# Performance work log

Measured on AMD Instinct MI355X. Metric: run time of the kernel, lower is better.

Reference implementation:

```python
import jax, jax.numpy as jnp
import numpy as np

B, N_TOK, C = 16, 4096, 512
TIME_DIM = 512
H_HEADS, WS = 8, 8
HEAD_DIM = C // H_HEADS
RES = 64  # sqrt(N_TOK)
NH = NW = RES // WS
SCALE = HEAD_DIM ** -0.5


def _rel_pos_index(ws):
    coords = np.stack(np.meshgrid(np.arange(ws), np.arange(ws), indexing='ij'))  # (2,ws,ws)
    flat = coords.reshape(2, -1)  # (2, ws*ws)
    rel = flat[:, :, None] - flat[:, None, :]  # (2, N, N)
    rel = rel.transpose(1, 2, 0).astype(np.int64)
    rel[:, :, 0] += ws - 1
    rel[:, :, 1] += ws - 1
    rel[:, :, 0] *= 2 * ws - 1
    return rel.sum(-1)  # (ws*ws, ws*ws)

REL_IDX = jnp.asarray(_rel_pos_index(WS))


def setup_inputs() -> dict:
    key = jax.random.key(0)
    ks = jax.random.split(key, 9)
    return {
        'x': jax.random.normal(ks[0], (B, N_TOK, C), jnp.float32),
        'time_emb': jax.random.normal(ks[1], (B, TIME_DIM), jnp.float32),
        'Wqkv': jax.random.normal(ks[2], (3 * C, C), jnp.float32) * 0.02,
        'bqkv': jnp.zeros((3 * C,), jnp.float32),
        'Wt': jax.random.normal(ks[3], (3 * C, TIME_DIM), jnp.float32) * 0.02,
        'bt': jnp.zeros((3 * C,), jnp.float32),
        'Wo': jax.random.normal(ks[4], (C, C), jnp.float32) * 0.02,
        'bo': jnp.zeros((C,), jnp.float32),
        'bias_table': jax.random.normal(ks[5], ((2 * WS - 1) ** 2, H_HEADS), jnp.float32) * 0.02,
    }


def reference(x, time_emb, Wqkv, bqkv, Wt, bt, Wo, bo, bias_table):
    Bo = x.shape[0]
    # window partition: (B, H*W, C) -> (B*nH*nW, ws*ws, C)
    xw = x.reshape(Bo, NH, WS, NW, WS, C).transpose(0, 1, 3, 2, 4, 5).reshape(-1, WS * WS, C)
    Bw, N = xw.shape[0], WS * WS
    # time emb broadcast to every window: (Bw, time_dim)
    te = jnp.broadcast_to(time_emb[:, None, :], (Bo, NH * NW, TIME_DIM)).reshape(Bw, TIME_DIM)
    # spatial qkv: (Bw, N, 3, h, d) -> q/k/v (Bw, h, N, d)
    qkv_s = (xw @ Wqkv.T + bqkv).reshape(Bw, N, 3, H_HEADS, HEAD_DIM).transpose(2, 0, 3, 1, 4)
    # time qkv: (Bw, 3, h, d) -> (3, Bw, h, 1, d)
    qkv_t = (te @ Wt.T + bt).reshape(Bw, 1, 3, H_HEADS, HEAD_DIM).transpose(2, 0, 3, 1, 4)
    q = qkv_s[0] + qkv_t[0]
    k = qkv_s[1] + qkv_t[1]
    v = qkv_s[2] + qkv_t[2]
    # relative position bias: (h, N, N)
    bias = bias_table[REL_IDX.reshape(-1)].reshape(N, N, H_HEADS).transpose(2, 0, 1)
    attn = jnp.einsum('bhnd,bhmd->bhnm', q, k) * SCALE + bias[None]
    attn = jax.nn.softmax(attn, axis=-1)
    out = jnp.einsum('bhnm,bhmd->bhnd', attn, v)
    out = out.transpose(0, 2, 1, 3).reshape(Bw, N, C)
    out = out @ Wo.T + bo
    # NOTE: source module's unpartition condition (ws^2 < ws^2) is False -> stays windowed
    return out
```

## Files before the change

kernel.cpp:

```cpp
#include <hip/hip_runtime.h>

using u16 = unsigned short;
typedef __bf16 bf16x8 __attribute__((ext_vector_type(8)));
typedef float floatx4 __attribute__((ext_vector_type(4)));

__device__ __forceinline__ u16 f2bf(float f) {
    union { float f; unsigned u; } v; v.f = f;
    unsigned r = v.u + 0x7fffu + ((v.u >> 16) & 1u);
    return (u16)(r >> 16);
}

__device__ __forceinline__ void gld16(const void* g, void* l) {
    __builtin_amdgcn_global_load_lds(
        (const __attribute__((address_space(1))) void*)g,
        (__attribute__((address_space(3))) void*)l, 16, 0, 0);
}

__device__ __forceinline__ void cvt4(const float* __restrict__ src,
                                     u16* __restrict__ dst, int i) {
    float4 v = *(const float4*)(src + i);
    ushort4 o;
    o.x = f2bf(v.x); o.y = f2bf(v.y); o.z = f2bf(v.z); o.w = f2bf(v.w);
    *(ushort4*)(dst + i) = o;
}

__global__ __launch_bounds__(256) void prep_k(
    const float* __restrict__ x, const float* __restrict__ Wqkv,
    const float* __restrict__ Wo, const float* __restrict__ te,
    const float* __restrict__ Wt, const float* __restrict__ bt,
    const float* __restrict__ btab,
    u16* __restrict__ xbf, u16* __restrict__ wqkvbf, u16* __restrict__ wobf,
    float* __restrict__ qkvt, float* __restrict__ biasf)
{
    const int b = blockIdx.x, tid = threadIdx.x;
    if (b < 768) {
        cvt4(Wqkv, wqkvbf, b * 1024 + tid * 4);
    } else if (b < 1024) {
        cvt4(Wo, wobf, (b - 768) * 1024 + tid * 4);
    } else if (b < 1120) {
        const int bb = b - 1024;
        const int batch = bb / 6;
        const int c = (bb % 6) * 256 + tid;
        const float4* a4 = (const float4*)(te + batch * 512);
        const float4* w4 = (const float4*)(Wt + (size_t)c * 512);
        float s = 0.f;
        for (int i = 0; i < 128; ++i) {
            float4 av = a4[i], wv = w4[i];
            s += av.x * wv.x + av.y * wv.y + av.z * wv.z + av.w * wv.w;
        }
        qkvt[batch * 1536 + c] = s + bt[c];
    } else if (b < 1152) {
        const int e0 = (b - 1120) * 1024 + tid;
        for (int k = 0; k < 4; ++k) {
            int e = e0 + k * 256;
            int h = e >> 12, rc = e & 4095, row = rc >> 6, col = rc & 63;
            int idx = ((row >> 3) - (col >> 3) + 7) * 15 + ((row & 7) - (col & 7) + 7);
            biasf[e] = btab[idx * 8 + h];
        }
    } else {
        const int base = (b - 1152) * 4096 + tid * 4;
        for (int k = 0; k < 4; ++k) cvt4(x, xbf, base + k * 1024);
    }
}

__global__ __launch_bounds__(256, 3) void gemm_qkv_k(
    const u16* __restrict__ A, const u16* __restrict__ B,
    const float* __restrict__ bqkv, const float* __restrict__ qkvt,
    u16* __restrict__ C)
{
    __shared__ __align__(16) u16 lA[128 * 32];
    __shared__ __align__(16) u16 lB[128 * 32];
    const int tid = threadIdx.x;
    const int lane = tid & 63, wv = tid >> 6;
    const int ln = lane & 15, quad = lane >> 4;
    const int tn = blockIdx.x, tm = blockIdx.y;
    const int wm = (wv & 1) * 64, wn = (wv >> 1) * 64;

    floatx4 acc[4][4];
#pragma unroll
    for (int i = 0; i < 4; ++i)
#pragma unroll
        for (int j = 0; j < 4; ++j) acc[i][j] = (floatx4){0.f, 0.f, 0.f, 0.f};

    const int srow = tid >> 2, scb = tid & 3;
    const u16* ag = A + (size_t)(tm * 128 + srow) * 512 + scb * 8;
    const u16* bg = B + (size_t)(tn * 128 + srow) * 512 + scb * 8;
    u16* la0 = &lA[tid * 8];
    u16* la1 = &lA[2048 + tid * 8];
    u16* lb0 = &lB[tid * 8];
    u16* lb1 = &lB[2048 + tid * 8];

    for (int k0 = 0; k0 < 512; k0 += 32) {
        __syncthreads();
        gld16(ag + k0, la0);
        gld16(ag + 64 * 512 + k0, la1);
        gld16(bg + k0, lb0);
        gld16(bg + 64 * 512 + k0, lb1);
        __syncthreads();
        bf16x8 af[4], bf[4];
#pragma unroll
        for (int mt = 0; mt < 4; ++mt)
            af[mt] = *(const bf16x8*)&lA[(wm + mt * 16 + ln) * 32 + quad * 8];
#pragma unroll
        for (int nt = 0; nt < 4; ++nt)
            bf[nt] = *(const bf16x8*)&lB[(wn + nt * 16 + ln) * 32 + quad * 8];
#pragma unroll
        for (int mt = 0; mt < 4; ++mt)
#pragma unroll
            for (int nt = 0; nt < 4; ++nt)
                acc[mt][nt] = __builtin_amdgcn_mfma_f32_16x16x32_bf16(
                    af[mt], bf[nt], acc[mt][nt], 0, 0, 0);
    }

    const float* qt = qkvt + (tm >> 5) * 1536;
#pragma unroll
    for (int nt = 0; nt < 4; ++nt) {
        const int col = tn * 128 + wn + nt * 16 + ln;
        const float add = bqkv[col] + qt[col];
#pragma unroll
        for (int mt = 0; mt < 4; ++mt) {
            const int row0 = tm * 128 + wm + mt * 16 + quad * 4;
#pragma unroll
            for (int r = 0; r < 4; ++r)
                C[(size_t)(row0 + r) * 1536 + col] = f2bf(acc[mt][nt][r] + add);
        }
    }
}

__global__ __launch_bounds__(256, 2) void attn_k(
    const u16* __restrict__ qkv, const float* __restrict__ biasf,
    u16* __restrict__ aout)
{
    __shared__ __align__(16) u16 vt[4][64 * 72];
    __shared__ __align__(16) u16 pl[4][64 * 72];
    const int tid = threadIdx.x, lane = tid & 63, wv = tid >> 6;
    const int ln = lane & 15, quad = lane >> 4;
    const int pair = blockIdx.x * 4 + wv;
    const int w = pair >> 3, h = pair & 7;
    const int bb = w >> 6, nh = (w >> 3) & 7, nw = w & 7;
    const int tbase = bb * 4096 + nh * 512 + nw * 8;
    u16* vtw = vt[wv];
    u16* plw = pl[wv];

    {
        const int wj = lane >> 3;
        const int d0 = (lane & 7) * 8;
#pragma unroll
        for (int i = 0; i < 8; ++i) {
            const int t = tbase + i * 64 + wj;
            union { bf16x8 v; u16 u[8]; } cv;
            cv.v = *(const bf16x8*)(qkv + (size_t)t * 1536 + 1024 + h * 64 + d0);
            const int n = i * 8 + wj;
#pragma unroll
            for (int j = 0; j < 8; ++j) vtw[(d0 + j) * 72 + n] = cv.u[j];
        }
    }

    bf16x8 kf[4][2];
#pragma unroll
    for (int nt = 0; nt < 4; ++nt) {
        const int n = nt * 16 + ln;
        const int t = tbase + (n >> 3) * 64 + (n & 7);
        const u16* kr = qkv + (size_t)t * 1536 + 512 + h * 64 + quad * 8;
        kf[nt][0] = *(const bf16x8*)kr;
        kf[nt][1] = *(const bf16x8*)(kr + 32);
    }

#pragma unroll
    for (int mt = 0; mt < 4; ++mt) {
        const int m = mt * 16 + ln;
        const int t = tbase + (m >> 3) * 64 + (m & 7);
        const u16* qr = qkv + (size_t)t * 1536 + h * 64 + quad * 8;
        const bf16x8 qf0 = *(const bf16x8*)qr;
        const bf16x8 qf1 = *(const bf16x8*)(qr + 32);
        floatx4 s[4];
#pragma unroll
        for (int nt = 0; nt < 4; ++nt) {
            s[nt] = (floatx4){0.f, 0.f, 0.f, 0.f};
            s[nt] = __builtin_amdgcn_mfma_f32_16x16x32_bf16(qf0, kf[nt][0], s[nt], 0, 0, 0);
            s[nt] = __builtin_amdgcn_mfma_f32_16x16x32_bf16(qf1, kf[nt][1], s[nt], 0, 0, 0);
        }
        float z[4][4];
        const float* bptr = biasf + h * 4096 + (mt * 16 + quad * 4) * 64 + ln;
#pragma unroll
        for (int nt = 0; nt < 4; ++nt)
#pragma unroll
            for (int r = 0; r < 4; ++r)
                z[nt][r] = s[nt][r] * 0.125f + bptr[r * 64 + nt * 16];
        float pmax[4], prcp[4];
#pragma unroll
        for (int r = 0; r < 4; ++r) {
            float v = fmaxf(fmaxf(z[0][r], z[1][r]), fmaxf(z[2][r], z[3][r]));
            v = fmaxf(v, __shfl_xor(v, 1));
            v = fmaxf(v, __shfl_xor(v, 2));
            v = fmaxf(v, __shfl_xor(v, 4));
            v = fmaxf(v, __shfl_xor(v, 8));
            pmax[r] = v;
        }
#pragma unroll
        for (int nt = 0; nt < 4; ++nt)
#pragma unroll
            for (int r = 0; r < 4; ++r)
                z[nt][r] = __expf(z[nt][r] - pmax[r]);
#pragma unroll
        for (int r = 0; r < 4; ++r) {
            float v = z[0][r] + z[1][r] + z[2][r] + z[3][r];
            v += __shfl_xor(v, 1);
            v += __shfl_xor(v, 2);
            v += __shfl_xor(v, 4);
            v += __shfl_xor(v, 8);
            prcp[r] = __builtin_amdgcn_rcpf(v);
        }
#pragma unroll
        for (int nt = 0; nt < 4; ++nt)
#pragma unroll
            for (int r = 0; r < 4; ++r)
                plw[(mt * 16 + quad * 4 + r) * 72 + nt * 16 + ln] =
                    f2bf(z[nt][r] * prcp[r]);
    }

    __syncthreads();

    bf16x8 vtf[4][2];
#pragma unroll
    for (int dt = 0; dt < 4; ++dt) {
        const u16* vr = &vtw[(dt * 16 + ln) * 72 + quad * 8];
        vtf[dt][0] = *(const bf16x8*)vr;
        vtf[dt][1] = *(const bf16x8*)(vr + 32);
    }
#pragma unroll
    for (int mt = 0; mt < 4; ++mt) {
        const u16* pr = &plw[(mt * 16 + ln) * 72 + quad * 8];
        const bf16x8 pf0 = *(const bf16x8*)pr;
        const bf16x8 pf1 = *(const bf16x8*)(pr + 32);
#pragma unroll
        for (int dt = 0; dt < 4; ++dt) {
            floatx4 o = (floatx4){0.f, 0.f, 0.f, 0.f};
            o = __builtin_amdgcn_mfma_f32_16x16x32_bf16(pf0, vtf[dt][0], o, 0, 0, 0);
            o = __builtin_amdgcn_mfma_f32_16x16x32_bf16(pf1, vtf[dt][1], o, 0, 0, 0);
            const size_t rbase =
                (size_t)(w * 64 + mt * 16 + quad * 4) * 512 + h * 64 + dt * 16 + ln;
#pragma unroll
            for (int r = 0; r < 4; ++r)
                aout[rbase + (size_t)r * 512] = f2bf(o[r]);
        }
    }
}

__global__ __launch_bounds__(256, 3) void gemm_out_k(
    const u16* __restrict__ A, const u16* __restrict__ B,
    const float* __restrict__ bo, float* __restrict__ C)
{
    __shared__ __align__(16) u16 lA[128 * 32];
    __shared__ __align__(16) u16 lB[128 * 32];
    const int tid = threadIdx.x;
    const int lane = tid & 63, wv = tid >> 6;
    const int ln = lane & 15, quad = lane >> 4;
    const int tn = blockIdx.x, tm = blockIdx.y;
    const int wm = (wv & 1) * 64, wn = (wv >> 1) * 64;

    floatx4 acc[4][4];
#pragma unroll
    for (int i = 0; i < 4; ++i)
#pragma unroll
        for (int j = 0; j < 4; ++j) acc[i][j] = (floatx4){0.f, 0.f, 0.f, 0.f};

    const int srow = tid >> 2, scb = tid & 3;
    const u16* ag = A + (size_t)(tm * 128 + srow) * 512 + scb * 8;
    const u16* bg = B + (size_t)(tn * 128 + srow) * 512 + scb * 8;
    u16* la0 = &lA[tid * 8];
    u16* la1 = &lA[2048 + tid * 8];
    u16* lb0 = &lB[tid * 8];
    u16* lb1 = &lB[2048 + tid * 8];

    for (int k0 = 0; k0 < 512; k0 += 32) {
        __syncthreads();
        gld16(ag + k0, la0);
        gld16(ag + 64 * 512 + k0, la1);
        gld16(bg + k0, lb0);
        gld16(bg + 64 * 512 + k0, lb1);
        __syncthreads();
        bf16x8 af[4], bf[4];
#pragma unroll
        for (int mt = 0; mt < 4; ++mt)
            af[mt] = *(const bf16x8*)&lA[(wm + mt * 16 + ln) * 32 + quad * 8];
#pragma unroll
        for (int nt = 0; nt < 4; ++nt)
            bf[nt] = *(const bf16x8*)&lB[(wn + nt * 16 + ln) * 32 + quad * 8];
#pragma unroll
        for (int mt = 0; mt < 4; ++mt)
#pragma unroll
            for (int nt = 0; nt < 4; ++nt)
                acc[mt][nt] = __builtin_amdgcn_mfma_f32_16x16x32_bf16(
                    af[mt], bf[nt], acc[mt][nt], 0, 0, 0);
    }

#pragma unroll
    for (int nt = 0; nt < 4; ++nt) {
        const int col = tn * 128 + wn + nt * 16 + ln;
        const float add = bo[col];
#pragma unroll
        for (int mt = 0; mt < 4; ++mt) {
            const int row0 = tm * 128 + wm + mt * 16 + quad * 4;
#pragma unroll
            for (int r = 0; r < 4; ++r)
                C[(size_t)(row0 + r) * 512 + col] = acc[mt][nt][r] + add;
        }
    }
}

extern "C" void kernel_launch(void* const* d_in, const int* in_sizes, int n_in,
                              void* d_out, int out_size, void* d_ws, size_t ws_size,
                              hipStream_t stream)
{
    const float* x    = (const float*)d_in[0];
    const float* te   = (const float*)d_in[1];
    const float* Wqkv = (const float*)d_in[2];
    const float* bqkv = (const float*)d_in[3];
    const float* Wt   = (const float*)d_in[4];
    const float* bt   = (const float*)d_in[5];
    const float* Wo   = (const float*)d_in[6];
    const float* bo   = (const float*)d_in[7];
    const float* btab = (const float*)d_in[8];
    float* out = (float*)d_out;

    char* w = (char*)d_ws;
    u16*   xbf    = (u16*)(w);
    u16*   qkvbf  = (u16*)(w + 67108864);
    u16*   wqkvbf = (u16*)(w + 268435456);
    u16*   wobf   = (u16*)(w + 270008320);
    float* qkvt   = (float*)(w + 270532608);
    float* biasf  = (float*)(w + 270630912);

    prep_k<<<9344, 256, 0, stream>>>(x, Wqkv, Wo, te, Wt, bt, btab,
                                     xbf, wqkvbf, wobf, qkvt, biasf);
    gemm_qkv_k<<<dim3(12, 512), 256, 0, stream>>>(xbf, wqkvbf, bqkv, qkvt, qkvbf);
    attn_k<<<2048, 256, 0, stream>>>(qkvbf, biasf, xbf );
    gemm_out_k<<<dim3(4, 512), 256, 0, stream>>>(xbf, wobf, bo, out);
}
```

Baseline: 510.2 us.

## Rewrite QKV GEMM as 256x256 tile, double-buffered, swizzled LDS pipeline

Replaces the simple 128x128 QKV projection GEMM, which synchronised twice per 32-wide K step, with a 256x256 tile using 512 threads. The new kernel double-buffers 64-wide K slices in LDS with XOR swizzling to avoid bank conflicts and interleaves global-to-LDS staging with MFMA phases using s_setprio and fine-grained waitcnt. It also remaps block IDs so neighbouring workgroups share data in cache. The larger tile raises reuse and hides load latency, at the cost of fewer workgroups (1536), one block per CU, and heavy register pressure.

```diff
diff --git a/kernel.cpp b/kernel.cpp
--- a/kernel.cpp
+++ b/kernel.cpp
@@ -63,63 +63,142 @@
     }
 }
 
-__global__ __launch_bounds__(256, 3) void gemm_qkv_k(
+#define MMQ(MB, NB, BF)                                                        \
+  _Pragma("unroll") for (int i_ = 0; i_ < 4; ++i_) {                           \
+    _Pragma("unroll") for (int j_ = 0; j_ < 2; ++j_) {                         \
+      acc[MB + i_][NB + j_] = __builtin_amdgcn_mfma_f32_16x16x32_bf16(         \
+          afr[i_][0], BF[j_][0], acc[MB + i_][NB + j_], 0, 0, 0);              \
+      acc[MB + i_][NB + j_] = __builtin_amdgcn_mfma_f32_16x16x32_bf16(         \
+          afr[i_][1], BF[j_][1], acc[MB + i_][NB + j_], 0, 0, 0);              \
+    }                                                                          \
+  }
+
+#define PHASES_TILE(BUF, S0, LASTIT)                                           \
+                \
+  LDA4(BUF, 0); LDB2(BUF, bf0, 0);                                             \
+  STAGE(S0 + 0);                                                               \
+  __builtin_amdgcn_s_barrier();                                                \
+  asm volatile("s_waitcnt lgkmcnt(0)" ::: "memory");                           \
+  __builtin_amdgcn_s_setprio(1);                                               \
+  MMQ(0, 0, bf0);                                                              \
+  __builtin_amdgcn_s_setprio(0);                                               \
+  __builtin_amdgcn_s_barrier();                                                \
+                          \
+  LDB2(BUF, bf1, 2);                                                           \
+  STAGE(S0 + 1);                                                               \
+  __builtin_amdgcn_s_barrier();                                                \
+  asm volatile("s_waitcnt lgkmcnt(0)" ::: "memory");                           \
+  __builtin_amdgcn_s_setprio(1);                                               \
+  MMQ(0, 2, bf1);                                                              \
+  __builtin_amdgcn_s_setprio(0);                                               \
+  __builtin_amdgcn_s_barrier();                                                \
+                          \
+  LDA4(BUF, 4);                                                                \
+  STAGE(S0 + 2);                                                               \
+  __builtin_amdgcn_s_barrier();                                                \
+  asm volatile("s_waitcnt lgkmcnt(0)" ::: "memory");                           \
+  __builtin_amdgcn_s_setprio(1);                                               \
+  MMQ(4, 2, bf1);                                                              \
+  __builtin_amdgcn_s_setprio(0);                                               \
+  __builtin_amdgcn_s_barrier();                                                \
+                   \
+  STAGE(S0 + 3);                                                               \
+  __builtin_amdgcn_s_barrier();                                                \
+  __builtin_amdgcn_s_setprio(1);                                               \
+  MMQ(4, 0, bf0);                                                              \
+  __builtin_amdgcn_s_setprio(0);                                               \
+  if (LASTIT) { asm volatile("s_waitcnt vmcnt(0)" ::: "memory"); }             \
+  else        { asm volatile("s_waitcnt vmcnt(2)" ::: "memory"); }             \
+  __builtin_amdgcn_s_barrier();
+
+__global__ __launch_bounds__(512, 1) void gemm_qkv_k(
     const u16* __restrict__ A, const u16* __restrict__ B,
     const float* __restrict__ bqkv, const float* __restrict__ qkvt,
     u16* __restrict__ C)
 {
-    __shared__ __align__(16) u16 lA[128 * 32];
-    __shared__ __align__(16) u16 lB[128 * 32];
+    __shared__ __align__(16) u16 lA[2 * 256 * 64];
+    __shared__ __align__(16) u16 lB[2 * 256 * 64];
     const int tid = threadIdx.x;
     const int lane = tid & 63, wv = tid >> 6;
     const int ln = lane & 15, quad = lane >> 4;
-    const int tn = blockIdx.x, tm = blockIdx.y;
-    const int wm = (wv & 1) * 64, wn = (wv >> 1) * 64;
-
-    floatx4 acc[4][4];
-#pragma unroll
-    for (int i = 0; i < 4; ++i)
+
+    const int orig = blockIdx.y * 6 + blockIdx.x;
+    const int wgid = (orig & 7) * 192 + (orig >> 3);
+    const int tm = wgid / 6, tn = wgid % 6;
+
+    const int wm = (wv >> 2) * 128;
+    const int wn = (wv & 3) * 64;
+
+    const u16* ag = A + (size_t)tm * 256 * 512;
+    const u16* bg = B + (size_t)tn * 256 * 512;
+
+    floatx4 acc[8][4];
+#pragma unroll
+    for (int i = 0; i < 8; ++i)
 #pragma unroll
         for (int j = 0; j < 4; ++j) acc[i][j] = (floatx4){0.f, 0.f, 0.f, 0.f};
 
-    const int srow = tid >> 2, scb = tid & 3;
-    const u16* ag = A + (size_t)(tm * 128 + srow) * 512 + scb * 8;
-    const u16* bg = B + (size_t)(tn * 128 + srow) * 512 + scb * 8;
-    u16* la0 = &lA[tid * 8];
-    u16* la1 = &lA[2048 + tid * 8];
-    u16* lb0 = &lB[tid * 8];
-    u16* lb1 = &lB[2048 + tid * 8];
-
-    for (int k0 = 0; k0 < 512; k0 += 32) {
-        __syncthreads();
-        gld16(ag + k0, la0);
-        gld16(ag + 64 * 512 + k0, la1);
-        gld16(bg + k0, lb0);
-        gld16(bg + 64 * 512 + k0, lb1);
-        __syncthreads();
-        bf16x8 af[4], bf[4];
-#pragma unroll
-        for (int mt = 0; mt < 4; ++mt)
-            af[mt] = *(const bf16x8*)&lA[(wm + mt * 16 + ln) * 32 + quad * 8];
-#pragma unroll
-        for (int nt = 0; nt < 4; ++nt)
-            bf[nt] = *(const bf16x8*)&lB[(wn + nt * 16 + ln) * 32 + quad * 8];
-#pragma unroll
-        for (int mt = 0; mt < 4; ++mt)
-#pragma unroll
-            for (int nt = 0; nt < 4; ++nt)
-                acc[mt][nt] = __builtin_amdgcn_mfma_f32_16x16x32_bf16(
-                    af[mt], bf[nt], acc[mt][nt], 0, 0, 0);
-    }
-
-    const float* qt = qkvt + (tm >> 5) * 1536;
+    bf16x8 afr[4][2];
+    bf16x8 bf0[2][2];
+    bf16x8 bf1[2][2];
+
+    auto STAGE = [&](int sidx) {
+        if (sidx >= 32) return;
+        const int h = sidx & 3, ts = sidx >> 2;
+        const u16* g = (h < 2) ? ag : bg;
+        u16* lb = ((h < 2) ? lA : lB) + (ts & 1) * (256 * 64);
+        const int r0 = (h & 1) * 128;
+        const int k0 = ts * 64;
+#pragma unroll
+        for (int rnd = 0; rnd < 2; ++rnd) {
+            const int r = r0 + rnd * 64 + (tid >> 3);
+            const int cb = ((tid & 7) * 16) ^ ((r & 7) << 4);
+            gld16(g + (size_t)r * 512 + k0 + (cb >> 1),
+                  lb + r * 64 + (tid & 7) * 8);
+        }
+    };
+
+    auto LDA4 = [&](int buf, int mb) {
+#pragma unroll
+        for (int i = 0; i < 4; ++i) {
+            const int r = wm + (mb + i) * 16 + ln;
+            const int sw = (r & 7) << 4;
+            const char* p = (const char*)(lA + buf * (256 * 64)) + r * 128;
+            afr[i][0] = *(const bf16x8*)(p + ((quad * 16) ^ sw));
+            afr[i][1] = *(const bf16x8*)(p + ((64 + quad * 16) ^ sw));
+        }
+    };
+    auto LDB2 = [&](int buf, bf16x8 (&bfr)[2][2], int nb) {
+#pragma unroll
+        for (int j = 0; j < 2; ++j) {
+            const int r = wn + (nb + j) * 16 + ln;
+            const int sw = (r & 7) << 4;
+            const char* p = (const char*)(lB + buf * (256 * 64)) + r * 128;
+            bfr[j][0] = *(const bf16x8*)(p + ((quad * 16) ^ sw));
+            bfr[j][1] = *(const bf16x8*)(p + ((64 + quad * 16) ^ sw));
+        }
+    };
+
+    STAGE(0); STAGE(1); STAGE(2); STAGE(3); STAGE(4);
+    asm volatile("s_waitcnt vmcnt(2)" ::: "memory");
+    __builtin_amdgcn_s_barrier();
+
+    int sidx = 5;
+    for (int it = 0; it < 4; ++it) {
+        const bool last = (it == 3);
+        PHASES_TILE(0, sidx + 0, last);
+        PHASES_TILE(1, sidx + 4, last);
+        sidx += 8;
+    }
+
+    const float* qt = qkvt + (tm >> 4) * 1536;
 #pragma unroll
     for (int nt = 0; nt < 4; ++nt) {
-        const int col = tn * 128 + wn + nt * 16 + ln;
+        const int col = tn * 256 + wn + nt * 16 + ln;
         const float add = bqkv[col] + qt[col];
 #pragma unroll
-        for (int mt = 0; mt < 4; ++mt) {
-            const int row0 = tm * 128 + wm + mt * 16 + quad * 4;
+        for (int mt = 0; mt < 8; ++mt) {
+            const int row0 = tm * 256 + wm + mt * 16 + quad * 4;
 #pragma unroll
             for (int r = 0; r < 4; ++r)
                 C[(size_t)(row0 + r) * 1536 + col] = f2bf(acc[mt][nt][r] + add);
@@ -334,7 +413,7 @@
 
     prep_k<<<9344, 256, 0, stream>>>(x, Wqkv, Wo, te, Wt, bt, btab,
                                      xbf, wqkvbf, wobf, qkvt, biasf);
-    gemm_qkv_k<<<dim3(12, 512), 256, 0, stream>>>(xbf, wqkvbf, bqkv, qkvt, qkvbf);
+    gemm_qkv_k<<<dim3(6, 256), 512, 0, stream>>>(xbf, wqkvbf, bqkv, qkvt, qkvbf);
     attn_k<<<2048, 256, 0, stream>>>(qkvbf, biasf, xbf );
     gemm_out_k<<<dim3(4, 512), 256, 0, stream>>>(xbf, wobf, bo, out);
 }
```

New measurement: 530.5 us. 1.04x slower.

## Fuse x conversion, QKV projection and window attention into one kernel

Applied to the files above, without the earlier changes.

Removes the separate x-to-bf16 pass and the QKV GEMM kernel. Each block now takes one window, converts its 64 tokens of x into LDS, and has each of its 8 waves compute its head's Q, K and V with MFMA, reading weights straight from global memory. Attention then runs on those register fragments. This avoids writing and re-reading the large bf16 qkv intermediate, but the weight tiles are loaded from global/L2 without LDS staging, and the 1024-block grid with large LDS per block may limit occupancy.

```diff
diff --git a/kernel.cpp b/kernel.cpp
--- a/kernel.cpp
+++ b/kernel.cpp
@@ -25,11 +25,10 @@
 }
 
 __global__ __launch_bounds__(256) void prep_k(
-    const float* __restrict__ x, const float* __restrict__ Wqkv,
-    const float* __restrict__ Wo, const float* __restrict__ te,
-    const float* __restrict__ Wt, const float* __restrict__ bt,
-    const float* __restrict__ btab,
-    u16* __restrict__ xbf, u16* __restrict__ wqkvbf, u16* __restrict__ wobf,
+    const float* __restrict__ Wqkv, const float* __restrict__ Wo,
+    const float* __restrict__ te, const float* __restrict__ Wt,
+    const float* __restrict__ bt, const float* __restrict__ btab,
+    u16* __restrict__ wqkvbf, u16* __restrict__ wobf,
     float* __restrict__ qkvt, float* __restrict__ biasf)
 {
     const int b = blockIdx.x, tid = threadIdx.x;
@@ -49,7 +48,7 @@
             s += av.x * wv.x + av.y * wv.y + av.z * wv.z + av.w * wv.w;
         }
         qkvt[batch * 1536 + c] = s + bt[c];
-    } else if (b < 1152) {
+    } else {
         const int e0 = (b - 1120) * 1024 + tid;
         for (int k = 0; k < 4; ++k) {
             int e = e0 + k * 256;
@@ -57,128 +56,112 @@
             int idx = ((row >> 3) - (col >> 3) + 7) * 15 + ((row & 7) - (col & 7) + 7);
             biasf[e] = btab[idx * 8 + h];
         }
-    } else {
-        const int base = (b - 1152) * 4096 + tid * 4;
-        for (int k = 0; k < 4; ++k) cvt4(x, xbf, base + k * 1024);
-    }
-}
-
-__global__ __launch_bounds__(256, 3) void gemm_qkv_k(
-    const u16* __restrict__ A, const u16* __restrict__ B,
+    }
+}
+
+
+#define GEMM64(CB)                                                             \
+  _Pragma("unroll") for (int i_ = 0; i_ < 4; ++i_)                             \
+    _Pragma("unroll") for (int j_ = 0; j_ < 4; ++j_)                           \
+      acc[i_][j_] = (floatx4){0.f, 0.f, 0.f, 0.f};                             \
+  _Pragma("unroll 2") for (int ks = 0; ks < 16; ++ks) {                        \
+    bf16x8 af_[4], bw_[4];                                                     \
+    _Pragma("unroll") for (int mt = 0; mt < 4; ++mt)                           \
+      af_[mt] = *(const bf16x8*)&xw[(mt * 16 + ln) * 520 + ks * 32 + quad * 8];\
+    _Pragma("unroll") for (int nt = 0; nt < 4; ++nt)                           \
+      bw_[nt] = *(const bf16x8*)(wqkv +                                        \
+          (size_t)((CB) + nt * 16 + ln) * 512 + ks * 32 + quad * 8);           \
+    _Pragma("unroll") for (int mt = 0; mt < 4; ++mt)                           \
+      _Pragma("unroll") for (int nt = 0; nt < 4; ++nt)                         \
+        acc[mt][nt] = __builtin_amdgcn_mfma_f32_16x16x32_bf16(                 \
+            af_[mt], bw_[nt], acc[mt][nt], 0, 0, 0);                           \
+  }
+
+#define WRN(CB)                                                                \
+  _Pragma("unroll") for (int nt = 0; nt < 4; ++nt) {                           \
+    const int col_ = (CB) + nt * 16 + ln;                                      \
+    const float add_ = bqkv[col_] + qtv[col_];                                 \
+    _Pragma("unroll") for (int mt = 0; mt < 4; ++mt)                           \
+      _Pragma("unroll") for (int r = 0; r < 4; ++r)                            \
+        buf[(mt * 16 + quad * 4 + r) * 72 + nt * 16 + ln] =                    \
+            f2bf(acc[mt][nt][r] + add_);                                       \
+  }
+
+#define WRT(CB)                                                                \
+  _Pragma("unroll") for (int nt = 0; nt < 4; ++nt) {                           \
+    const int col_ = (CB) + nt * 16 + ln;                                      \
+    const float add_ = bqkv[col_] + qtv[col_];                                 \
+    _Pragma("unroll") for (int mt = 0; mt < 4; ++mt)                           \
+      _Pragma("unroll") for (int r = 0; r < 4; ++r)                            \
+        buf[(nt * 16 + ln) * 72 + mt * 16 + quad * 4 + r] =                    \
+            f2bf(acc[mt][nt][r] + add_);                                       \
+  }
+
+#define RDF(DST)                                                               \
+  _Pragma("unroll") for (int i_ = 0; i_ < 4; ++i_) {                           \
+    const u16* p_ = &buf[(i_ * 16 + ln) * 72 + quad * 8];                      \
+    DST[i_][0] = *(const bf16x8*)p_;                                           \
+    DST[i_][1] = *(const bf16x8*)(p_ + 32);                                    \
+  }
+
+__global__ __launch_bounds__(512, 2) void fused_k(
+    const float* __restrict__ x, const u16* __restrict__ wqkv,
     const float* __restrict__ bqkv, const float* __restrict__ qkvt,
-    u16* __restrict__ C)
+    const float* __restrict__ biasf, u16* __restrict__ aout)
 {
-    __shared__ __align__(16) u16 lA[128 * 32];
-    __shared__ __align__(16) u16 lB[128 * 32];
-    const int tid = threadIdx.x;
-    const int lane = tid & 63, wv = tid >> 6;
-    const int ln = lane & 15, quad = lane >> 4;
-    const int tn = blockIdx.x, tm = blockIdx.y;
-    const int wm = (wv & 1) * 64, wn = (wv >> 1) * 64;
-
-    floatx4 acc[4][4];
-#pragma unroll
-    for (int i = 0; i < 4; ++i)
-#pragma unroll
-        for (int j = 0; j < 4; ++j) acc[i][j] = (floatx4){0.f, 0.f, 0.f, 0.f};
-
-    const int srow = tid >> 2, scb = tid & 3;
-    const u16* ag = A + (size_t)(tm * 128 + srow) * 512 + scb * 8;
-    const u16* bg = B + (size_t)(tn * 128 + srow) * 512 + scb * 8;
-    u16* la0 = &lA[tid * 8];
-    u16* la1 = &lA[2048 + tid * 8];
-    u16* lb0 = &lB[tid * 8];
-    u16* lb1 = &lB[2048 + tid * 8];
-
-    for (int k0 = 0; k0 < 512; k0 += 32) {
-        __syncthreads();
-        gld16(ag + k0, la0);
-        gld16(ag + 64 * 512 + k0, la1);
-        gld16(bg + k0, lb0);
-        gld16(bg + 64 * 512 + k0, lb1);
-        __syncthreads();
-        bf16x8 af[4], bf[4];
-#pragma unroll
-        for (int mt = 0; mt < 4; ++mt)
-            af[mt] = *(const bf16x8*)&lA[(wm + mt * 16 + ln) * 32 + quad * 8];
-#pragma unroll
-        for (int nt = 0; nt < 4; ++nt)
-            bf[nt] = *(const bf16x8*)&lB[(wn + nt * 16 + ln) * 32 + quad * 8];
-#pragma unroll
-        for (int mt = 0; mt < 4; ++mt)
-#pragma unroll
-            for (int nt = 0; nt < 4; ++nt)
-                acc[mt][nt] = __builtin_amdgcn_mfma_f32_16x16x32_bf16(
-                    af[mt], bf[nt], acc[mt][nt], 0, 0, 0);
-    }
-
-    const float* qt = qkvt + (tm >> 5) * 1536;
-#pragma unroll
-    for (int nt = 0; nt < 4; ++nt) {
-        const int col = tn * 128 + wn + nt * 16 + ln;
-        const float add = bqkv[col] + qt[col];
-#pragma unroll
-        for (int mt = 0; mt < 4; ++mt) {
-            const int row0 = tm * 128 + wm + mt * 16 + quad * 4;
-#pragma unroll
-            for (int r = 0; r < 4; ++r)
-                C[(size_t)(row0 + r) * 1536 + col] = f2bf(acc[mt][nt][r] + add);
-        }
-    }
-}
-
-__global__ __launch_bounds__(256, 2) void attn_k(
-    const u16* __restrict__ qkv, const float* __restrict__ biasf,
-    u16* __restrict__ aout)
-{
-    __shared__ __align__(16) u16 vt[4][64 * 72];
-    __shared__ __align__(16) u16 pl[4][64 * 72];
+    __shared__ __align__(16) u16 xw[64 * 520];
+    __shared__ __align__(16) u16 sbuf[8][64 * 72];
     const int tid = threadIdx.x, lane = tid & 63, wv = tid >> 6;
     const int ln = lane & 15, quad = lane >> 4;
-    const int pair = blockIdx.x * 4 + wv;
-    const int w = pair >> 3, h = pair & 7;
+    const int w = blockIdx.x;
     const int bb = w >> 6, nh = (w >> 3) & 7, nw = w & 7;
     const int tbase = bb * 4096 + nh * 512 + nw * 8;
-    u16* vtw = vt[wv];
-    u16* plw = pl[wv];
+    const int h = wv;
+    u16* buf = sbuf[wv];
+    const float* qtv = qkvt + bb * 1536;
 
     {
-        const int wj = lane >> 3;
-        const int d0 = (lane & 7) * 8;
-#pragma unroll
-        for (int i = 0; i < 8; ++i) {
-            const int t = tbase + i * 64 + wj;
-            union { bf16x8 v; u16 u[8]; } cv;
-            cv.v = *(const bf16x8*)(qkv + (size_t)t * 1536 + 1024 + h * 64 + d0);
-            const int n = i * 8 + wj;
-#pragma unroll
-            for (int j = 0; j < 8; ++j) vtw[(d0 + j) * 72 + n] = cv.u[j];
-        }
-    }
-
-    bf16x8 kf[4][2];
-#pragma unroll
-    for (int nt = 0; nt < 4; ++nt) {
-        const int n = nt * 16 + ln;
-        const int t = tbase + (n >> 3) * 64 + (n & 7);
-        const u16* kr = qkv + (size_t)t * 1536 + 512 + h * 64 + quad * 8;
-        kf[nt][0] = *(const bf16x8*)kr;
-        kf[nt][1] = *(const bf16x8*)(kr + 32);
-    }
+        const int t = tid >> 3, cc = tid & 7;
+        const int g = tbase + (t >> 3) * 64 + (t & 7);
+        const float* xr = x + (size_t)g * 512;
+        u16* dst = &xw[t * 520];
+#pragma unroll
+        for (int c = 0; c < 8; ++c) {
+            const int col = cc * 8 + c * 64;
+            float4 a = *(const float4*)(xr + col);
+            float4 bvec = *(const float4*)(xr + col + 4);
+            ushort4 lo, hi;
+            lo.x = f2bf(a.x); lo.y = f2bf(a.y); lo.z = f2bf(a.z); lo.w = f2bf(a.w);
+            hi.x = f2bf(bvec.x); hi.y = f2bf(bvec.y); hi.z = f2bf(bvec.z); hi.w = f2bf(bvec.w);
+            *(ushort4*)(dst + col) = lo;
+            *(ushort4*)(dst + col + 4) = hi;
+        }
+    }
+    __syncthreads();
+
+    floatx4 acc[4][4];
+    bf16x8 qf[4][2], kf[4][2], vtf[4][2];
+
+    GEMM64(h * 64);
+    WRN(h * 64);
+    RDF(qf);
+
+    GEMM64(512 + h * 64);
+    WRN(512 + h * 64);
+    RDF(kf);
+
+    GEMM64(1024 + h * 64);
+    WRT(1024 + h * 64);
+    RDF(vtf);
 
 #pragma unroll
     for (int mt = 0; mt < 4; ++mt) {
-        const int m = mt * 16 + ln;
-        const int t = tbase + (m >> 3) * 64 + (m & 7);
-        const u16* qr = qkv + (size_t)t * 1536 + h * 64 + quad * 8;
-        const bf16x8 qf0 = *(const bf16x8*)qr;
-        const bf16x8 qf1 = *(const bf16x8*)(qr + 32);
         floatx4 s[4];
 #pragma unroll
         for (int nt = 0; nt < 4; ++nt) {
             s[nt] = (floatx4){0.f, 0.f, 0.f, 0.f};
-            s[nt] = __builtin_amdgcn_mfma_f32_16x16x32_bf16(qf0, kf[nt][0], s[nt], 0, 0, 0);
-            s[nt] = __builtin_amdgcn_mfma_f32_16x16x32_bf16(qf1, kf[nt][1], s[nt], 0, 0, 0);
+            s[nt] = __builtin_amdgcn_mfma_f32_16x16x32_bf16(qf[mt][0], kf[nt][0], s[nt], 0, 0, 0);
+            s[nt] = __builtin_amdgcn_mfma_f32_16x16x32_bf16(qf[mt][1], kf[nt][1], s[nt], 0, 0, 0);
         }
         float z[4][4];
         const float* bptr = biasf + h * 4096 + (mt * 16 + quad * 4) * 64 + ln;
@@ -215,22 +198,13 @@
         for (int nt = 0; nt < 4; ++nt)
 #pragma unroll
             for (int r = 0; r < 4; ++r)
-                plw[(mt * 16 + quad * 4 + r) * 72 + nt * 16 + ln] =
+                buf[(mt * 16 + quad * 4 + r) * 72 + nt * 16 + ln] =
                     f2bf(z[nt][r] * prcp[r]);
     }
 
-    __syncthreads();
-
-    bf16x8 vtf[4][2];
-#pragma unroll
-    for (int dt = 0; dt < 4; ++dt) {
-        const u16* vr = &vtw[(dt * 16 + ln) * 72 + quad * 8];
-        vtf[dt][0] = *(const bf16x8*)vr;
-        vtf[dt][1] = *(const bf16x8*)(vr + 32);
-    }
 #pragma unroll
     for (int mt = 0; mt < 4; ++mt) {
-        const u16* pr = &plw[(mt * 16 + ln) * 72 + quad * 8];
+        const u16* pr = &buf[(mt * 16 + ln) * 72 + quad * 8];
         const bf16x8 pf0 = *(const bf16x8*)pr;
         const bf16x8 pf1 = *(const bf16x8*)(pr + 32);
 #pragma unroll
@@ -325,16 +299,14 @@
     float* out = (float*)d_out;
 
     char* w = (char*)d_ws;
-    u16*   xbf    = (u16*)(w);
-    u16*   qkvbf  = (u16*)(w + 67108864);
+    u16*   aoutbf = (u16*)(w);
     u16*   wqkvbf = (u16*)(w + 268435456);
     u16*   wobf   = (u16*)(w + 270008320);
     float* qkvt   = (float*)(w + 270532608);
     float* biasf  = (float*)(w + 270630912);
 
-    prep_k<<<9344, 256, 0, stream>>>(x, Wqkv, Wo, te, Wt, bt, btab,
-                                     xbf, wqkvbf, wobf, qkvt, biasf);
-    gemm_qkv_k<<<dim3(12, 512), 256, 0, stream>>>(xbf, wqkvbf, bqkv, qkvt, qkvbf);
-    attn_k<<<2048, 256, 0, stream>>>(qkvbf, biasf, xbf );
-    gemm_out_k<<<dim3(4, 512), 256, 0, stream>>>(xbf, wobf, bo, out);
-}
+    prep_k<<<1152, 256, 0, stream>>>(Wqkv, Wo, te, Wt, bt, btab,
+                                     wqkvbf, wobf, qkvt, biasf);
+    fused_k<<<1024, 512, 0, stream>>>(x, wqkvbf, bqkv, qkvt, biasf, aoutbf);
+    gemm_out_k<<<dim3(4, 512), 256, 0, stream>>>(aoutbf, wobf, bo, out);
+}
```

Result: no change. 506.3 us (-0.8%).

## Fuse window attention with output projection and swizzle QKV GEMM block order

Applied to the files above, without the earlier changes.

Merges the attention kernel and the output-projection GEMM into one kernel. Each 512-thread block handles one window with all 8 heads, stages the attention output for that window in LDS, and multiplies it by Wo read straight from global memory with register double-buffering. This removes the bf16 round trip of the attention output through global memory and one kernel launch. The QKV GEMM also gets a block-index remap to improve cache locality, and s_setprio hints are added around the MFMA sections. In exchange, occupancy drops to one large block per CU, and each block reloads all of Wo without LDS staging.

```diff
diff --git a/kernel.cpp b/kernel.cpp
--- a/kernel.cpp
+++ b/kernel.cpp
@@ -73,7 +73,11 @@
     const int tid = threadIdx.x;
     const int lane = tid & 63, wv = tid >> 6;
     const int ln = lane & 15, quad = lane >> 4;
-    const int tn = blockIdx.x, tm = blockIdx.y;
+
+    const int orig = blockIdx.y * 12 + blockIdx.x;
+    const int wgid = (orig & 7) * 768 + (orig >> 3);
+    const int tm = wgid / 12, tn = wgid % 12;
+
     const int wm = (wv & 1) * 64, wn = (wv >> 1) * 64;
 
     floatx4 acc[4][4];
@@ -127,20 +131,20 @@
     }
 }
 
-__global__ __launch_bounds__(256, 2) void attn_k(
+__global__ __launch_bounds__(512, 1) void attn_out_k(
     const u16* __restrict__ qkv, const float* __restrict__ biasf,
-    u16* __restrict__ aout)
+    const u16* __restrict__ wo, const float* __restrict__ bo,
+    float* __restrict__ out)
 {
-    __shared__ __align__(16) u16 vt[4][64 * 72];
-    __shared__ __align__(16) u16 pl[4][64 * 72];
+    __shared__ __align__(16) u16 ab[64 * 520];
+    __shared__ __align__(16) u16 sbuf[8][64 * 72];
     const int tid = threadIdx.x, lane = tid & 63, wv = tid >> 6;
     const int ln = lane & 15, quad = lane >> 4;
-    const int pair = blockIdx.x * 4 + wv;
-    const int w = pair >> 3, h = pair & 7;
+    const int w = blockIdx.x;
     const int bb = w >> 6, nh = (w >> 3) & 7, nw = w & 7;
     const int tbase = bb * 4096 + nh * 512 + nw * 8;
-    u16* vtw = vt[wv];
-    u16* plw = pl[wv];
+    const int h = wv;
+    u16* buf = sbuf[wv];
 
     {
         const int wj = lane >> 3;
@@ -152,8 +156,16 @@
             cv.v = *(const bf16x8*)(qkv + (size_t)t * 1536 + 1024 + h * 64 + d0);
             const int n = i * 8 + wj;
 #pragma unroll
-            for (int j = 0; j < 8; ++j) vtw[(d0 + j) * 72 + n] = cv.u[j];
-        }
+            for (int j = 0; j < 8; ++j) buf[(d0 + j) * 72 + n] = cv.u[j];
+        }
+    }
+
+    bf16x8 vtf[4][2];
+#pragma unroll
+    for (int dt = 0; dt < 4; ++dt) {
+        const u16* vr = &buf[(dt * 16 + ln) * 72 + quad * 8];
+        vtf[dt][0] = *(const bf16x8*)vr;
+        vtf[dt][1] = *(const bf16x8*)(vr + 32);
     }
 
     bf16x8 kf[4][2];
@@ -174,12 +186,14 @@
         const bf16x8 qf0 = *(const bf16x8*)qr;
         const bf16x8 qf1 = *(const bf16x8*)(qr + 32);
         floatx4 s[4];
+        __builtin_amdgcn_s_setprio(1);
 #pragma unroll
         for (int nt = 0; nt < 4; ++nt) {
             s[nt] = (floatx4){0.f, 0.f, 0.f, 0.f};
             s[nt] = __builtin_amdgcn_mfma_f32_16x16x32_bf16(qf0, kf[nt][0], s[nt], 0, 0, 0);
             s[nt] = __builtin_amdgcn_mfma_f32_16x16x32_bf16(qf1, kf[nt][1], s[nt], 0, 0, 0);
         }
+        __builtin_amdgcn_s_setprio(0);
         float z[4][4];
         const float* bptr = biasf + h * 4096 + (mt * 16 + quad * 4) * 64 + ln;
 #pragma unroll
@@ -215,96 +229,92 @@
         for (int nt = 0; nt < 4; ++nt)
 #pragma unroll
             for (int r = 0; r < 4; ++r)
-                plw[(mt * 16 + quad * 4 + r) * 72 + nt * 16 + ln] =
+                buf[(mt * 16 + quad * 4 + r) * 72 + nt * 16 + ln] =
                     f2bf(z[nt][r] * prcp[r]);
     }
 
-    __syncthreads();
-
-    bf16x8 vtf[4][2];
-#pragma unroll
-    for (int dt = 0; dt < 4; ++dt) {
-        const u16* vr = &vtw[(dt * 16 + ln) * 72 + quad * 8];
-        vtf[dt][0] = *(const bf16x8*)vr;
-        vtf[dt][1] = *(const bf16x8*)(vr + 32);
-    }
 #pragma unroll
     for (int mt = 0; mt < 4; ++mt) {
-        const u16* pr = &plw[(mt * 16 + ln) * 72 + quad * 8];
+        const u16* pr = &buf[(mt * 16 + ln) * 72 + quad * 8];
         const bf16x8 pf0 = *(const bf16x8*)pr;
         const bf16x8 pf1 = *(const bf16x8*)(pr + 32);
 #pragma unroll
         for (int dt = 0; dt < 4; ++dt) {
             floatx4 o = (floatx4){0.f, 0.f, 0.f, 0.f};
+            __builtin_amdgcn_s_setprio(1);
             o = __builtin_amdgcn_mfma_f32_16x16x32_bf16(pf0, vtf[dt][0], o, 0, 0, 0);
             o = __builtin_amdgcn_mfma_f32_16x16x32_bf16(pf1, vtf[dt][1], o, 0, 0, 0);
-            const size_t rbase =
-                (size_t)(w * 64 + mt * 16 + quad * 4) * 512 + h * 64 + dt * 16 + ln;
-#pragma unroll
-            for (int r = 0; r < 4; ++r)
-                aout[rbase + (size_t)r * 512] = f2bf(o[r]);
-        }
-    }
-}
-
-__global__ __launch_bounds__(256, 3) void gemm_out_k(
-    const u16* __restrict__ A, const u16* __restrict__ B,
-    const float* __restrict__ bo, float* __restrict__ C)
-{
-    __shared__ __align__(16) u16 lA[128 * 32];
-    __shared__ __align__(16) u16 lB[128 * 32];
-    const int tid = threadIdx.x;
-    const int lane = tid & 63, wv = tid >> 6;
-    const int ln = lane & 15, quad = lane >> 4;
-    const int tn = blockIdx.x, tm = blockIdx.y;
-    const int wm = (wv & 1) * 64, wn = (wv >> 1) * 64;
+            __builtin_amdgcn_s_setprio(0);
+#pragma unroll
+            for (int r = 0; r < 4; ++r)
+                ab[(mt * 16 + quad * 4 + r) * 520 + h * 64 + dt * 16 + ln] =
+                    f2bf(o[r]);
+        }
+    }
+
+    __syncthreads();
 
     floatx4 acc[4][4];
 #pragma unroll
     for (int i = 0; i < 4; ++i)
 #pragma unroll
         for (int j = 0; j < 4; ++j) acc[i][j] = (floatx4){0.f, 0.f, 0.f, 0.f};
-
-    const int srow = tid >> 2, scb = tid & 3;
-    const u16* ag = A + (size_t)(tm * 128 + srow) * 512 + scb * 8;
-    const u16* bg = B + (size_t)(tn * 128 + srow) * 512 + scb * 8;
-    u16* la0 = &lA[tid * 8];
-    u16* la1 = &lA[2048 + tid * 8];
-    u16* lb0 = &lB[tid * 8];
-    u16* lb1 = &lB[2048 + tid * 8];
-
-    for (int k0 = 0; k0 < 512; k0 += 32) {
-        __syncthreads();
-        gld16(ag + k0, la0);
-        gld16(ag + 64 * 512 + k0, la1);
-        gld16(bg + k0, lb0);
-        gld16(bg + 64 * 512 + k0, lb1);
-        __syncthreads();
-        bf16x8 af[4], bf[4];
+    const u16* wb = wo + (size_t)(wv * 64 + ln) * 512 + quad * 8;
+
+    bf16x8 aX[4], bX[4], aY[4], bY[4];
+#pragma unroll
+    for (int mt = 0; mt < 4; ++mt)
+        aX[mt] = *(const bf16x8*)&ab[(mt * 16 + ln) * 520 + quad * 8];
+#pragma unroll
+    for (int nt = 0; nt < 4; ++nt)
+        bX[nt] = *(const bf16x8*)(wb + (size_t)nt * 16 * 512);
+
+#pragma unroll
+    for (int ks = 0; ks < 16; ks += 2) {
+        if (ks + 1 < 16) {
+#pragma unroll
+            for (int mt = 0; mt < 4; ++mt)
+                aY[mt] = *(const bf16x8*)&ab[(mt * 16 + ln) * 520 + (ks + 1) * 32 + quad * 8];
+#pragma unroll
+            for (int nt = 0; nt < 4; ++nt)
+                bY[nt] = *(const bf16x8*)(wb + (size_t)nt * 16 * 512 + (ks + 1) * 32);
+        }
+        __builtin_amdgcn_s_setprio(1);
 #pragma unroll
         for (int mt = 0; mt < 4; ++mt)
-            af[mt] = *(const bf16x8*)&lA[(wm + mt * 16 + ln) * 32 + quad * 8];
-#pragma unroll
-        for (int nt = 0; nt < 4; ++nt)
-            bf[nt] = *(const bf16x8*)&lB[(wn + nt * 16 + ln) * 32 + quad * 8];
+#pragma unroll
+            for (int nt = 0; nt < 4; ++nt)
+                acc[mt][nt] = __builtin_amdgcn_mfma_f32_16x16x32_bf16(
+                    aX[mt], bX[nt], acc[mt][nt], 0, 0, 0);
+        __builtin_amdgcn_s_setprio(0);
+        if (ks + 2 < 16) {
+#pragma unroll
+            for (int mt = 0; mt < 4; ++mt)
+                aX[mt] = *(const bf16x8*)&ab[(mt * 16 + ln) * 520 + (ks + 2) * 32 + quad * 8];
+#pragma unroll
+            for (int nt = 0; nt < 4; ++nt)
+                bX[nt] = *(const bf16x8*)(wb + (size_t)nt * 16 * 512 + (ks + 2) * 32);
+        }
+        __builtin_amdgcn_s_setprio(1);
 #pragma unroll
         for (int mt = 0; mt < 4; ++mt)
 #pragma unroll
             for (int nt = 0; nt < 4; ++nt)
                 acc[mt][nt] = __builtin_amdgcn_mfma_f32_16x16x32_bf16(
-                    af[mt], bf[nt], acc[mt][nt], 0, 0, 0);
+                    aY[mt], bY[nt], acc[mt][nt], 0, 0, 0);
+        __builtin_amdgcn_s_setprio(0);
     }
 
 #pragma unroll
     for (int nt = 0; nt < 4; ++nt) {
-        const int col = tn * 128 + wn + nt * 16 + ln;
+        const int col = wv * 64 + nt * 16 + ln;
         const float add = bo[col];
 #pragma unroll
         for (int mt = 0; mt < 4; ++mt) {
-            const int row0 = tm * 128 + wm + mt * 16 + quad * 4;
-#pragma unroll
-            for (int r = 0; r < 4; ++r)
-                C[(size_t)(row0 + r) * 512 + col] = acc[mt][nt][r] + add;
+            const int row0 = w * 64 + mt * 16 + quad * 4;
+#pragma unroll
+            for (int r = 0; r < 4; ++r)
+                out[(size_t)(row0 + r) * 512 + col] = acc[mt][nt][r] + add;
         }
     }
 }
@@ -335,6 +345,5 @@
     prep_k<<<9344, 256, 0, stream>>>(x, Wqkv, Wo, te, Wt, bt, btab,
                                      xbf, wqkvbf, wobf, qkvt, biasf);
     gemm_qkv_k<<<dim3(12, 512), 256, 0, stream>>>(xbf, wqkvbf, bqkv, qkvt, qkvbf);
-    attn_k<<<2048, 256, 0, stream>>>(qkvbf, biasf, xbf );
-    gemm_out_k<<<dim3(4, 512), 256, 0, stream>>>(xbf, wobf, bo, out);
-}
+    attn_out_k<<<1024, 512, 0, stream>>>(qkvbf, biasf, wobf, bo, out);
+}
```

Result: slower. 523.3 us (+2.6%).
